# Performance work log

Hardware: AMD Instinct MI355X
Metric: run time of the kernel (lower is better)

Reference implementation:

```python
import jax, jax.numpy as jnp
import numpy as np

# Irreps: 0e+1e+2e+3e -> spherical dims per irrep = 2l+1 = [1,3,5,7], total dim 16.
# One allowed path per irrep (l_in==l_out, same parity), num_paths = 4.
# path_norm: one path per output irrep -> factor 1/sqrt(1) = 1 (no-op).
IRREP_DIMS = [1, 3, 5, 7]
N_NODES = 50000
C_IN = 128
C_OUT = 128


def setup_inputs() -> dict:
    key = jax.random.key(0)
    k1, k2 = jax.random.split(key)
    x = jax.random.normal(k1, (N_NODES, sum(IRREP_DIMS), C_IN), dtype=jnp.float32)
    # linear init scaled by 1/sqrt(channels_in), as in initialize_linear
    weight = jax.random.normal(k2, (len(IRREP_DIMS), C_IN, C_OUT), dtype=jnp.float32) / np.sqrt(C_IN)
    # map spherical index m -> path index
    seg_ids = jnp.asarray(np.repeat(np.arange(len(IRREP_DIMS)), IRREP_DIMS), dtype=jnp.int32)
    return {"x": x, "weight": weight, "seg_ids": seg_ids}


def reference(x, weight, seg_ids):
    # Block-diagonal equivariant linear: for each spherical component m,
    # out[n, m, :] = x[n, m, :] @ weight[path(m)].
    # and contract in a single batched GEMM.
    w_m = weight[seg_ids]                      # (M, C_in, C_out)
    out = jnp.einsum('nmc,mcd->nmd', x, w_m)   # (N, M, C_out)
    return out
```

## Files before the change

kernel.cpp:

```cpp
#include <hip/hip_runtime.h>
#include <stdint.h>


typedef __attribute__((ext_vector_type(8))) short short8;
typedef __attribute__((ext_vector_type(4))) float floatx4;

static __device__ __forceinline__ unsigned short f2bf(float f) {
    uint32_t u = __builtin_bit_cast(uint32_t, f);
    uint32_t r = (u + 0x7FFFu + ((u >> 16) & 1u)) >> 16;
    return (unsigned short)r;
}

__global__ void pack_weights_kernel(const float* __restrict__ w,
                                    unsigned short* __restrict__ wp) {
    int tid = blockIdx.x * 256 + threadIdx.x;
    int j    = tid & 7;
    int lane = (tid >> 3) & 63;
    int kt   = (tid >> 9) & 3;
    int dt   = (tid >> 11) & 7;
    int s    = (tid >> 14) & 3;
    int c = kt * 32 + (lane >> 4) * 8 + j;
    int d = dt * 16 + (lane & 15);
    wp[tid] = f2bf(w[((size_t)s * 128 + c) * 128 + d]);
}

__global__ __launch_bounds__(256, 2) void irreps_main_kernel(
    const float* __restrict__ x, const unsigned short* __restrict__ wp,
    const int* __restrict__ seg_ids, float* __restrict__ out)
{
    const int lane   = threadIdx.x & 63;
    const int waveId = blockIdx.x * 4 + (threadIdx.x >> 6);
    const int m      = waveId >> 7;
    const int w_in_m = waveId & 127;
    const int seg    = seg_ids[m];
    const int q      = lane >> 4;
    const int ln15   = lane & 15;

    short8 B[8][4];
    {
        const unsigned short* wb = wp + ((size_t)seg << 14);
        #pragma unroll
        for (int dt = 0; dt < 8; ++dt)
            #pragma unroll
            for (int kt = 0; kt < 4; ++kt)
                B[dt][kt] = *(const short8*)(wb + (((dt * 4 + kt) * 64 + lane) << 3));
    }

    for (int t = w_in_m; t < 3125; t += 128) {
        const int node0 = t << 4;
        const float* xr = x + (((size_t)(node0 + ln15) * 16 + m) << 7) + q * 8;

        floatx4 f[8];
        #pragma unroll
        for (int kt = 0; kt < 4; ++kt) {
            f[2 * kt]     = *(const floatx4*)(xr + kt * 32);
            f[2 * kt + 1] = *(const floatx4*)(xr + kt * 32 + 4);
        }

        short8 A[4];
        #pragma unroll
        for (int kt = 0; kt < 4; ++kt) {
            short8 a;
            #pragma unroll
            for (int e = 0; e < 4; ++e) a[e]     = (short)f2bf(f[2 * kt][e]);
            #pragma unroll
            for (int e = 0; e < 4; ++e) a[e + 4] = (short)f2bf(f[2 * kt + 1][e]);
            A[kt] = a;
        }

        floatx4 acc[8];
        #pragma unroll
        for (int dt = 0; dt < 8; ++dt) acc[dt] = (floatx4){0.f, 0.f, 0.f, 0.f};

        #pragma unroll
        for (int kt = 0; kt < 4; ++kt)
            #pragma unroll
            for (int dt = 0; dt < 8; ++dt)
                acc[dt] = __builtin_amdgcn_mfma_f32_16x16x32_bf16(
                    A[kt], B[dt][kt], acc[dt], 0, 0, 0);

        float* ob = out + (((size_t)node0 * 16 + m) << 7) + ln15;
        #pragma unroll
        for (int i = 0; i < 4; ++i) {
            float* orow = ob + (size_t)(q * 4 + i) * 2048;
            #pragma unroll
            for (int dt = 0; dt < 8; ++dt) orow[dt * 16] = acc[dt][i];
        }
    }
}

extern "C" void kernel_launch(void* const* d_in, const int* in_sizes, int n_in,
                              void* d_out, int out_size, void* d_ws, size_t ws_size,
                              hipStream_t stream) {
    const float* x   = (const float*)d_in[0];
    const float* w   = (const float*)d_in[1];
    const int*   seg = (const int*)d_in[2];
    float* out = (float*)d_out;
    unsigned short* wp = (unsigned short*)d_ws;

    hipLaunchKernelGGL(pack_weights_kernel, dim3(256), dim3(256), 0, stream, w, wp);
    hipLaunchKernelGGL(irreps_main_kernel, dim3(512), dim3(256), 0, stream,
                       x, wp, seg, out);
}
```

Baseline: 668.5 us.

## Stage x loads and output stores through swizzled LDS for coalesced access

```diff
diff --git a/kernel.cpp b/kernel.cpp
--- a/kernel.cpp
+++ b/kernel.cpp
@@ -3,6 +3,7 @@
 
 
 typedef __attribute__((ext_vector_type(8))) short short8;
+typedef __attribute__((ext_vector_type(4))) short sh4;
 typedef __attribute__((ext_vector_type(4))) float floatx4;
 
 static __device__ __forceinline__ unsigned short f2bf(float f) {
@@ -28,13 +29,21 @@
     const float* __restrict__ x, const unsigned short* __restrict__ wp,
     const int* __restrict__ seg_ids, float* __restrict__ out)
 {
-    const int lane   = threadIdx.x & 63;
-    const int waveId = blockIdx.x * 4 + (threadIdx.x >> 6);
+    __shared__ char lds_all[4][12 * 1024];
+
+    const int lane = threadIdx.x & 63;
+    const int wib  = threadIdx.x >> 6;
+    char* const xa = lds_all[wib];
+    char* const ob = lds_all[wib] + 4096;
+
+    const int waveId = blockIdx.x * 4 + wib;
     const int m      = waveId >> 7;
     const int w_in_m = waveId & 127;
     const int seg    = seg_ids[m];
     const int q      = lane >> 4;
     const int ln15   = lane & 15;
+    const int nsub   = lane >> 5;
+    const int c16    = lane & 31;
 
     short8 B[8][4];
     {
@@ -46,27 +55,31 @@
                 B[dt][kt] = *(const short8*)(wb + (((dt * 4 + kt) * 64 + lane) << 3));
     }
 
+    int xa_rd[4];
+    #pragma unroll
+    for (int kt = 0; kt < 4; ++kt)
+        xa_rd[kt] = ln15 * 256 + ((kt * 64 + q * 16) ^ ((ln15 & 7) << 4));
+
     for (int t = w_in_m; t < 3125; t += 128) {
         const int node0 = t << 4;
-        const float* xr = x + (((size_t)(node0 + ln15) * 16 + m) << 7) + q * 8;
 
-        floatx4 f[8];
         #pragma unroll
-        for (int kt = 0; kt < 4; ++kt) {
-            f[2 * kt]     = *(const floatx4*)(xr + kt * 32);
-            f[2 * kt + 1] = *(const floatx4*)(xr + kt * 32 + 4);
+        for (int r = 0; r < 8; ++r) {
+            const int node = 2 * r + nsub;
+            const float* gp = x + (((size_t)(node0 + node) * 16 + m) << 7) + c16 * 4;
+            floatx4 v = *(const floatx4*)gp;
+            sh4 h;
+            h[0] = (short)f2bf(v[0]);
+            h[1] = (short)f2bf(v[1]);
+            h[2] = (short)f2bf(v[2]);
+            h[3] = (short)f2bf(v[3]);
+            *(sh4*)(xa + node * 256 + ((c16 * 8) ^ ((node & 7) << 4))) = h;
         }
 
         short8 A[4];
         #pragma unroll
-        for (int kt = 0; kt < 4; ++kt) {
-            short8 a;
-            #pragma unroll
-            for (int e = 0; e < 4; ++e) a[e]     = (short)f2bf(f[2 * kt][e]);
-            #pragma unroll
-            for (int e = 0; e < 4; ++e) a[e + 4] = (short)f2bf(f[2 * kt + 1][e]);
-            A[kt] = a;
-        }
+        for (int kt = 0; kt < 4; ++kt)
+            A[kt] = *(const short8*)(xa + xa_rd[kt]);
 
         floatx4 acc[8];
         #pragma unroll
@@ -79,12 +92,23 @@
                 acc[dt] = __builtin_amdgcn_mfma_f32_16x16x32_bf16(
                     A[kt], B[dt][kt], acc[dt], 0, 0, 0);
 
-        float* ob = out + (((size_t)node0 * 16 + m) << 7) + ln15;
         #pragma unroll
         for (int i = 0; i < 4; ++i) {
-            float* orow = ob + (size_t)(q * 4 + i) * 2048;
+            const int row = q * 4 + i;
+            char* rp = ob + row * 512;
+            const int sw = (row & 7) << 4;
             #pragma unroll
-            for (int dt = 0; dt < 8; ++dt) orow[dt * 16] = acc[dt][i];
+            for (int dt = 0; dt < 8; ++dt)
+                *(float*)(rp + ((dt * 64 + ln15 * 4) ^ sw)) = acc[dt][i];
+        }
+
+        #pragma unroll
+        for (int p = 0; p < 8; ++p) {
+            const int node = 2 * p + nsub;
+            floatx4 v = *(const floatx4*)(ob + node * 512 +
+                                          ((c16 * 16) ^ ((node & 7) << 4)));
+            float* gp = out + (((size_t)(node0 + node) * 16 + m) << 7) + c16 * 4;
+            *(floatx4*)gp = v;
         }
     }
 }
```

Measured after the change: 645.9 us. 3.4% less time.
